# Kernel tuning notes

Measured on AMD Instinct MI355X. Metric: run time of the kernel, lower is better.

The kernel has to match this reference:

```python
import jax, jax.numpy as jnp
import numpy as np

VOC_SIZE = 32768
DIM = 512
NUM_TOPK = 64
BATCH = 4096


def setup_inputs() -> dict:
    key = jax.random.key(0)
    ks = jax.random.split(key, 8)
    lim = 1.0 / np.sqrt(DIM)  # kaiming_uniform(a=sqrt(5)) on [V, d] -> U(-1/sqrt(d), 1/sqrt(d))
    x = jax.random.normal(ks[0], (BATCH, DIM), dtype=jnp.float32)
    codebook = jax.random.uniform(ks[1], (VOC_SIZE, DIM), dtype=jnp.float32, minval=-lim, maxval=lim)
    Wq = jax.random.uniform(ks[2], (DIM, DIM), dtype=jnp.float32, minval=-lim, maxval=lim)
    bq = jax.random.uniform(ks[3], (DIM,), dtype=jnp.float32, minval=-lim, maxval=lim)
    Wk = jax.random.uniform(ks[4], (DIM, DIM), dtype=jnp.float32, minval=-lim, maxval=lim)
    bk = jax.random.uniform(ks[5], (DIM,), dtype=jnp.float32, minval=-lim, maxval=lim)
    Wv = jax.random.uniform(ks[6], (DIM, DIM), dtype=jnp.float32, minval=-lim, maxval=lim)
    bv = jax.random.uniform(ks[7], (DIM,), dtype=jnp.float32, minval=-lim, maxval=lim)
    return {"x": x, "codebook": codebook, "Wq": Wq, "bq": bq,
            "Wk": Wk, "bk": bk, "Wv": Wv, "bv": bv}


def reference(x, codebook, Wq, bq, Wk, bk, Wv, bv):
    # projections (torch Linear with weight stored pre-transposed as [in, out])
    q = x @ Wq + bq              # [B, d]
    k = codebook @ Wk + bk       # [V, d]
    v = codebook @ Wv + bv       # [V, d]

    dots = jnp.einsum('bd,kd->bk', q, k)              # [B, V]
    top, _ = jax.lax.top_k(dots, NUM_TOPK)            # [B, num_topk]
    thresh = top[..., -1:]                            # k-th largest value per row
    mask_value = -jnp.finfo(dots.dtype).max
    dots = jnp.where(dots < thresh, mask_value, dots)
    attn = jax.nn.softmax(dots, axis=-1)              # [B, V]
    out = jnp.einsum('bk,kd->bd', attn, v)            # [B, d]
    return out
```

## Files before the change

kernel.cpp:

```cpp
#include <hip/hip_runtime.h>
#include <cstdint>

#define VOC   32768
#define DIM   512
#define TOPK  64
#define BATCH 4096

#define KSIG     2.45f
#define EPS_SEL  0.012f
#define CAND_CAP 512
#define RES_CAP  256
#define FCAP     1024

typedef unsigned short u16;
typedef __attribute__((ext_vector_type(8))) short bf16x8;
typedef __attribute__((ext_vector_type(4))) float f32x4;

__device__ __forceinline__ u16 f2bf(float f) {
    unsigned u = __float_as_uint(f);
    unsigned r = (u + 0x7FFFu + ((u >> 16) & 1u)) >> 16;
    return (u16)r;
}
__device__ __forceinline__ float bf2f(u16 h) {
    return __uint_as_float(((unsigned)h) << 16);
}
__device__ __forceinline__ unsigned enc16(u16 h) {
    return (h & 0x8000u) ? (unsigned)((u16)~h) : (unsigned)(h | 0x8000u);
}
__device__ __forceinline__ float dec16(unsigned s16) {
    u16 h = (s16 & 0x8000u) ? (u16)(s16 ^ 0x8000u) : (u16)(~s16);
    return bf2f(h);
}

__device__ __forceinline__ void async16(const void* g, void* l) {
    __builtin_amdgcn_global_load_lds(
        (const __attribute__((address_space(1))) void*)g,
        (__attribute__((address_space(3))) void*)l, 16, 0, 0);
}

template <bool BT, bool F64ACC>
__global__ __launch_bounds__(256)
void gemm64(const float* __restrict__ A, const float* __restrict__ B,
            const float* __restrict__ bias, float* __restrict__ C,
            int M, int N, int K)
{
    const int KS = 16;
    __shared__ float As[KS][68];
    __shared__ float Bs[KS][64];

    const int tid = threadIdx.x;
    const int m0 = blockIdx.y * 64;
    const int n0 = blockIdx.x * 64;
    const int ty = tid >> 4;
    const int tx = tid & 15;

    float acc[4][4];
    double acc64[4][4];
#pragma unroll
    for (int i = 0; i < 4; i++)
#pragma unroll
        for (int j = 0; j < 4; j++) { acc[i][j] = 0.f; if (F64ACC) acc64[i][j] = 0.0; }

    for (int kt = 0; kt < K; kt += KS) {
        {
            int row = tid >> 2, kq = tid & 3;
            const float4 av = *(const float4*)(A + (size_t)(m0 + row) * K + kt + kq * 4);
            As[kq * 4 + 0][row] = av.x;
            As[kq * 4 + 1][row] = av.y;
            As[kq * 4 + 2][row] = av.z;
            As[kq * 4 + 3][row] = av.w;
        }
        if (!BT) {
            int krow = tid >> 4, nq = tid & 15;
            *(float4*)&Bs[krow][nq * 4] =
                *(const float4*)(B + (size_t)(kt + krow) * N + n0 + nq * 4);
        } else {
            int nrow = tid >> 2, kq = tid & 3;
            const float4 bv = *(const float4*)(B + (size_t)(n0 + nrow) * K + kt + kq * 4);
            Bs[kq * 4 + 0][nrow] = bv.x;
            Bs[kq * 4 + 1][nrow] = bv.y;
            Bs[kq * 4 + 2][nrow] = bv.z;
            Bs[kq * 4 + 3][nrow] = bv.w;
        }
        __syncthreads();

#pragma unroll
        for (int kk = 0; kk < KS; kk++) {
            float4 a = *(const float4*)&As[kk][ty * 4];
            float4 b = *(const float4*)&Bs[kk][tx * 4];
            float av[4] = {a.x, a.y, a.z, a.w};
            float bv[4] = {b.x, b.y, b.z, b.w};
#pragma unroll
            for (int i = 0; i < 4; i++)
#pragma unroll
                for (int j = 0; j < 4; j++)
                    acc[i][j] += av[i] * bv[j];
        }
        __syncthreads();
        if (F64ACC) {
#pragma unroll
            for (int i = 0; i < 4; i++)
#pragma unroll
                for (int j = 0; j < 4; j++) { acc64[i][j] += (double)acc[i][j]; acc[i][j] = 0.f; }
        }
    }

    float4 bb = make_float4(0.f, 0.f, 0.f, 0.f);
    if (bias) bb = *(const float4*)(bias + n0 + tx * 4);
#pragma unroll
    for (int i = 0; i < 4; i++) {
        float4 o;
        o.x = (F64ACC ? (float)acc64[i][0] : acc[i][0]) + bb.x;
        o.y = (F64ACC ? (float)acc64[i][1] : acc[i][1]) + bb.y;
        o.z = (F64ACC ? (float)acc64[i][2] : acc[i][2]) + bb.z;
        o.w = (F64ACC ? (float)acc64[i][3] : acc[i][3]) + bb.w;
        *(float4*)(C + (size_t)(m0 + ty * 4 + i) * N + n0 + tx * 4) = o;
    }
}

__global__ void bias_fold(const float* __restrict__ bq, const float* __restrict__ Wk,
                          float* __restrict__ bqk)
{
    int j = blockIdx.x * 256 + threadIdx.x;
    if (j >= DIM) return;
    double s = 0.0;
    const float* wr = Wk + (size_t)j * DIM;
    for (int d = 0; d < DIM; d++) s += (double)bq[d] * (double)wr[d];
    bqk[j] = (float)s;
}

__global__ void zero_ws(unsigned* __restrict__ p, int n)
{
    int i = blockIdx.x * 256 + threadIdx.x;
    if (i < n) p[i] = 0u;
}

__global__ __launch_bounds__(256)
void cbar_accum(const float* __restrict__ cb, float* __restrict__ cbarsum)
{
    const int tid = threadIdx.x;
    const int r0 = blockIdx.x * 128;
    float s0 = 0.f, s1 = 0.f;
    for (int r = 0; r < 128; r++) {
        const float* rp = cb + (size_t)(r0 + r) * DIM;
        s0 += rp[tid];
        s1 += rp[tid + 256];
    }
    atomicAdd(&cbarsum[tid], s0);
    atomicAdd(&cbarsum[tid + 256], s1);
}

__global__ __launch_bounds__(256)
void rowstats(const float* __restrict__ q2, const float* __restrict__ cbarsum,
              float* __restrict__ trow, float* __restrict__ sigrow)
{
    const int tid = threadIdx.x, lane = tid & 63, wave = tid >> 6;
    const int row = blockIdx.x * 4 + wave;
    const float* qp = q2 + (size_t)row * DIM + lane * 8;
    float4 a0 = *(const float4*)qp, a1 = *(const float4*)(qp + 4);
    const float* cp = cbarsum + lane * 8;
    float4 c0 = *(const float4*)cp, c1 = *(const float4*)(cp + 4);
    float mu = a0.x*c0.x + a0.y*c0.y + a0.z*c0.z + a0.w*c0.w
             + a1.x*c1.x + a1.y*c1.y + a1.z*c1.z + a1.w*c1.w;
    float nr = a0.x*a0.x + a0.y*a0.y + a0.z*a0.z + a0.w*a0.w
             + a1.x*a1.x + a1.y*a1.y + a1.z*a1.z + a1.w*a1.w;
#pragma unroll
    for (int off = 32; off > 0; off >>= 1) {
        mu += __shfl_down(mu, off);
        nr += __shfl_down(nr, off);
    }
    if (lane == 0) {
        mu *= (1.f / VOC);
        float sig = sqrtf(nr * (1.f / 1536.f));
        trow[row] = mu + KSIG * sig;
        sigrow[row] = sig;
    }
}

__global__ __launch_bounds__(256)
void pack_rows(const float* __restrict__ src, u16* __restrict__ hi,
               u16* __restrict__ lo, int R, int log2R)
{
    int idx = blockIdx.x * 256 + threadIdx.x;
    int c8  = idx >> log2R;
    int row = idx & (R - 1);
    const float* sp = src + (size_t)row * DIM + c8 * 8;
    float xv[8];
    *(float4*)&xv[0] = *(const float4*)sp;
    *(float4*)&xv[4] = *(const float4*)(sp + 4);
    int ks = c8 >> 2, ch = c8 & 3;
    size_t ob = ((size_t)(ks * 4 + ch) * R + row) * 8;
    u16 h[8], l[8];
#pragma unroll
    for (int j = 0; j < 8; j++) {
        h[j] = f2bf(xv[j]);
        l[j] = f2bf(xv[j] - bf2f(h[j]));
    }
    *(uint4*)(hi + ob) = *(const uint4*)h;
    if (lo) *(uint4*)(lo + ob) = *(const uint4*)l;
}

__global__ __launch_bounds__(256)
void pack_bT(const float* __restrict__ W, u16* __restrict__ hi, u16* __restrict__ lo)
{
    int idx = blockIdx.x * 256 + threadIdx.x;
    int n  = idx & (DIM - 1);
    int c8 = idx >> 9;
    int ks = c8 >> 2, ch = c8 & 3;
    size_t ob = ((size_t)(ks * 4 + ch) * DIM + n) * 8;
    u16 h[8], l[8];
#pragma unroll
    for (int j = 0; j < 8; j++) {
        float x = W[(size_t)(c8 * 8 + j) * DIM + n];
        h[j] = f2bf(x);
        l[j] = f2bf(x - bf2f(h[j]));
    }
    *(uint4*)(hi + ob) = *(const uint4*)h;
    *(uint4*)(lo + ob) = *(const uint4*)l;
}

__global__ __launch_bounds__(256, 3)
void mfma_dots(const u16* __restrict__ Ah, const u16* __restrict__ Bh,
               const float* __restrict__ trow, unsigned* __restrict__ candBuf,
               unsigned* __restrict__ counters)
{
    __shared__ u16 lds[3 * 8192];

    const int tid  = threadIdx.x;
    const int lane = tid & 63;
    const int wave = tid >> 6;
    const int wm = wave >> 1, wn = wave & 1;
    const int lr = lane & 15;
    const int q  = lane >> 4;

    const int L   = blockIdx.x;
    const int xcd = L & 7;
    const int j   = L >> 3;
    const int m0  = (xcd * 4 + (j & 3)) * 128;
    const int n0  = (j >> 2) * 128;

    const int a  = wave >> 1;
    const u16* src = a ? Bh : Ah;
    const int rb   = a ? n0 : m0;
    const size_t R = a ? (size_t)VOC : (size_t)BATCH;
    const int i0   = (wave & 1) * 4;

    f32x4 acc[4][4] = {};

#define ISSUE(ks, b)                                                          \
    {                                                                         \
        _Pragma("unroll")                                                     \
        for (int s_ = 0; s_ < 4; s_++) {                                      \
            int i_ = i0 + s_;                                                 \
            const u16* gp_ = src + ((size_t)((ks) * 4 + (i_ >> 1)) * R + rb   \
                                    + (i_ & 1) * 64 + lane) * 8;              \
            async16(gp_, &lds[(b) * 8192 + a * 4096 + i_ * 512 + lane * 8]);  \
        }                                                                     \
    }

    ISSUE(0, 0)
    ISSUE(1, 1)

    for (int s = 0; s < 16; s++) {
        if (s == 15) __builtin_amdgcn_s_waitcnt(0x0F70);
        else         __builtin_amdgcn_s_waitcnt(0x0F74);
        __builtin_amdgcn_s_barrier();
        if (s < 14) {
            int b2 = (s + 2) % 3;
            ISSUE(s + 2, b2)
        }
        const u16* base = &lds[(s % 3) * 8192];

        bf16x8 ah[4];
#pragma unroll
        for (int mt = 0; mt < 4; mt++)
            ah[mt] = *(const bf16x8*)&base[q * 1024 + (wm * 64 + mt * 16 + lr) * 8];
#pragma unroll
        for (int nt = 0; nt < 4; nt++) {
            bf16x8 bh = *(const bf16x8*)&base[4096 + q * 1024 + (wn * 64 + nt * 16 + lr) * 8];
#pragma unroll
            for (int mt = 0; mt < 4; mt++)
                acc[mt][nt] = __builtin_amdgcn_mfma_f32_16x16x32_bf16(ah[mt], bh, acc[mt][nt], 0, 0, 0);
        }
    }
#undef ISSUE

#pragma unroll
    for (int mt = 0; mt < 4; mt++) {
#pragma unroll
        for (int r = 0; r < 4; r++) {
            int rowg = m0 + wm * 64 + mt * 16 + q * 4 + r;
            float tr = trow[rowg];
#pragma unroll
            for (int nt = 0; nt < 4; nt++) {
                float val = acc[mt][nt][r];
                if (val >= tr) {
                    unsigned slot = atomicAdd(&counters[rowg], 1u);
                    if (slot < CAND_CAP) {
                        unsigned s16 = enc16(f2bf(val));
                        candBuf[(size_t)rowg * CAND_CAP + slot] =
                            (s16 << 16) | (unsigned)(n0 + wn * 64 + nt * 16 + lr);
                    }
                }
            }
        }
    }
}

__global__ __launch_bounds__(256, 2)
void mfma_out(const u16* __restrict__ Ah, const u16* __restrict__ Al,
              const u16* __restrict__ Bh, const u16* __restrict__ Bl,
              const float* __restrict__ bias, float* __restrict__ Cout, int Ma)
{
    __shared__ u16 lds[2 * 16384];

    const int tid  = threadIdx.x;
    const int lane = tid & 63;
    const int wave = tid >> 6;
    const int wm = wave >> 1, wn = wave & 1;
    const int m0 = blockIdx.y * 128, n0 = blockIdx.x * 128;
    const int lr = lane & 15;
    const int q  = lane >> 4;

    f32x4 acc[4][4] = {};
    const u16* garr[4] = {Ah, Bh, Al, Bl};
    const int a = wave;
    const u16* src = garr[a];
    const bool isA = (a == 0 || a == 2);
    const int rb = isA ? m0 : n0;
    const size_t R = isA ? (size_t)Ma : (size_t)DIM;

#define VISSUE(ks, b)                                                         \
    {                                                                         \
        _Pragma("unroll")                                                     \
        for (int i_ = 0; i_ < 8; i_++) {                                      \
            const u16* gp_ = src + ((size_t)((ks) * 4 + (i_ >> 1)) * R + rb   \
                                    + (i_ & 1) * 64 + lane) * 8;              \
            async16(gp_, &lds[(b) * 16384 + a * 4096 + i_ * 512 + lane * 8]); \
        }                                                                     \
    }

    VISSUE(0, 0)

    for (int ks = 0; ks < 16; ks++) {
        __syncthreads();
        if (ks < 15) VISSUE(ks + 1, (ks + 1) & 1)
        const u16* base = &lds[(ks & 1) * 16384];

        bf16x8 ah[4], al[4];
#pragma unroll
        for (int mt = 0; mt < 4; mt++) {
            int row = wm * 64 + mt * 16 + lr;
            ah[mt] = *(const bf16x8*)&base[0 * 4096 + q * 1024 + row * 8];
            al[mt] = *(const bf16x8*)&base[2 * 4096 + q * 1024 + row * 8];
        }
#pragma unroll
        for (int nt = 0; nt < 4; nt++) {
            int col = wn * 64 + nt * 16 + lr;
            bf16x8 bh = *(const bf16x8*)&base[1 * 4096 + q * 1024 + col * 8];
            bf16x8 bl = *(const bf16x8*)&base[3 * 4096 + q * 1024 + col * 8];
#pragma unroll
            for (int mt = 0; mt < 4; mt++) {
                acc[mt][nt] = __builtin_amdgcn_mfma_f32_16x16x32_bf16(ah[mt], bh, acc[mt][nt], 0, 0, 0);
                acc[mt][nt] = __builtin_amdgcn_mfma_f32_16x16x32_bf16(ah[mt], bl, acc[mt][nt], 0, 0, 0);
                acc[mt][nt] = __builtin_amdgcn_mfma_f32_16x16x32_bf16(al[mt], bh, acc[mt][nt], 0, 0, 0);
            }
        }
    }
#undef VISSUE

#pragma unroll
    for (int mt = 0; mt < 4; mt++)
#pragma unroll
        for (int nt = 0; nt < 4; nt++) {
            int col = n0 + wn * 64 + nt * 16 + lr;
            float bb = bias[col];
#pragma unroll
            for (int r = 0; r < 4; r++) {
                int rowg = m0 + wm * 64 + mt * 16 + q * 4 + r;
                Cout[(size_t)rowg * DIM + col] = acc[mt][nt][r] + bb;
            }
        }
}

__global__ __launch_bounds__(256)
void select6(const unsigned* __restrict__ candBuf, const unsigned* __restrict__ counters,
             const float* __restrict__ trow, const float* __restrict__ q2,
             const float* __restrict__ codebook, float* __restrict__ y,
             unsigned* __restrict__ flags)
{
    __shared__ unsigned recs[CAND_CAP];
    __shared__ unsigned long long keys[RES_CAP];
    __shared__ float q2s[DIM];
    __shared__ float wArr[RES_CAP];
    __shared__ float redf[256];
    __shared__ unsigned redu[256];
    __shared__ unsigned s_R;

    const int tid  = threadIdx.x;
    const int lane = tid & 63;
    const int wave = tid >> 6;
    const int row  = blockIdx.x;

    const unsigned cnt = counters[row];
    if (cnt < TOPK || cnt > CAND_CAP) {
        if (tid == 0) flags[row] = 1u;
        return;
    }
    for (int i = tid; i < DIM; i += 256) q2s[i] = q2[(size_t)row * DIM + i];
    for (int i = tid; i < CAND_CAP; i += 256)
        recs[i] = (i < (int)cnt) ? candBuf[(size_t)row * CAND_CAP + i] : 0u;
    if (tid == 0) s_R = 0;
    __syncthreads();

    for (int k = 2; k <= CAND_CAP; k <<= 1) {
        for (int j = k >> 1; j > 0; j >>= 1) {
#pragma unroll
            for (int e = 0; e < 2; e++) {
                int i = tid + e * 256;
                int ixj = i ^ j;
                if (ixj > i) {
                    unsigned a = recs[i], b = recs[ixj];
                    if (((i & k) == 0) ? (a < b) : (a > b)) { recs[i] = b; recs[ixj] = a; }
                }
            }
            __syncthreads();
        }
    }

    const float a64  = dec16(recs[TOPK - 1] >> 16);
    const float band = a64 - 2.f * EPS_SEL;
    if (trow[row] > band) {
        if (tid == 0) flags[row] = 1u;
        return;
    }

#pragma unroll
    for (int e = 0; e < 2; e++) {
        int i = tid + e * 256;
        if (i < (int)cnt && dec16(recs[i] >> 16) >= band) atomicAdd(&s_R, 1u);
    }
    __syncthreads();
    const int R = (int)s_R;
    if (R > RES_CAP) {
        if (tid == 0) flags[row] = 1u;
        return;
    }

    for (int c = wave; c < R; c += 4) {
        unsigned idx = recs[c] & 0xFFFFu;
        const float* cb = codebook + (size_t)idx * DIM + lane * 8;
        float4 c0 = *(const float4*)cb, c1 = *(const float4*)(cb + 4);
        const float* qp = &q2s[lane * 8];
        float4 a0 = *(const float4*)qp, a1 = *(const float4*)(qp + 4);
        double s = (double)a0.x * c0.x + (double)a0.y * c0.y
                 + (double)a0.z * c0.z + (double)a0.w * c0.w
                 + (double)a1.x * c1.x + (double)a1.y * c1.y
                 + (double)a1.z * c1.z + (double)a1.w * c1.w;
#pragma unroll
        for (int off = 32; off > 0; off >>= 1) s += __shfl_down(s, off);
        if (lane == 0) {
            float val = (float)s;
            unsigned b = __float_as_uint(val);
            unsigned sk = (b & 0x80000000u) ? ~b : (b | 0x80000000u);
            keys[c] = ((unsigned long long)(~sk) << 32) | idx;
        }
    }
    if (tid >= R && tid < RES_CAP) keys[tid] = ~0ULL;
    __syncthreads();

    for (int k = 2; k <= RES_CAP; k <<= 1) {
        for (int j = k >> 1; j > 0; j >>= 1) {
            int ixj = tid ^ j;
            if (ixj > tid) {
                unsigned long long a = keys[tid], b2 = keys[ixj];
                if (((tid & k) == 0) ? (a > b2) : (a < b2)) { keys[tid] = b2; keys[ixj] = a; }
            }
            __syncthreads();
        }
    }

    const unsigned threshInv = (unsigned)(keys[TOPK - 1] >> 32);
    unsigned sk0 = ~(unsigned)(keys[0] >> 32);
    const float vmax = __uint_as_float((sk0 & 0x80000000u) ? (sk0 & 0x7FFFFFFFu) : ~sk0);

    unsigned hi = (unsigned)(keys[tid] >> 32);
    bool sel = (hi <= threshInv);
    unsigned sk = ~hi;
    float val = __uint_as_float((sk & 0x80000000u) ? (sk & 0x7FFFFFFFu) : ~sk);
    float w = sel ? expf(val - vmax) : 0.f;
    wArr[tid] = w;
    redf[tid] = w;
    redu[tid] = sel ? 1u : 0u;
    __syncthreads();
    for (int s = 128; s > 0; s >>= 1) {
        if (tid < s) { redf[tid] += redf[tid + s]; redu[tid] += redu[tid + s]; }
        __syncthreads();
    }
    const float invZ = 1.0f / redf[0];
    const int selCount = (int)redu[0];

    for (int d = tid; d < DIM; d += 256) {
        float acc = 0.f;
        for (int i = 0; i < selCount; i++) {
            unsigned idx = (unsigned)(keys[i] & 0xFFFFFFFFu);
            acc += wArr[i] * codebook[(size_t)idx * DIM + d];
        }
        y[(size_t)row * DIM + d] = acc * invZ;
    }
}

__global__ __launch_bounds__(256)
void fallback_row(const unsigned* __restrict__ flags, const float* __restrict__ q2,
                  const float* __restrict__ codebook, const float* __restrict__ trow,
                  const float* __restrict__ sigrow, float* __restrict__ y)
{
    const int row = blockIdx.x;
    if (!flags[row]) return;

    __shared__ float q2s[DIM];
    __shared__ unsigned long long keys[FCAP];
    __shared__ float wArr[FCAP];
    __shared__ float redf[256];
    __shared__ unsigned redu[256];
    __shared__ unsigned s_cnt;

    const int tid = threadIdx.x;
    for (int i = tid; i < DIM; i += 256) q2s[i] = q2[(size_t)row * DIM + i];
    const float sig = sigrow[row];
    float tf = trow[row] - 0.35f * sig;
    unsigned cnt = 0;

    for (int it = 0; it < 16; it++) {
        if (tid == 0) s_cnt = 0;
        __syncthreads();
        for (int i = tid; i < VOC; i += 256) {
            const float* cb = codebook + (size_t)i * DIM;
            double s = 0.0;
            for (int d = 0; d < DIM; d += 4) {
                float4 c4 = *(const float4*)(cb + d);
                s += (double)q2s[d + 0] * (double)c4.x + (double)q2s[d + 1] * (double)c4.y
                   + (double)q2s[d + 2] * (double)c4.z + (double)q2s[d + 3] * (double)c4.w;
            }
            float vv = (float)s;
            if (vv >= tf) {
                unsigned p = atomicAdd(&s_cnt, 1u);
                if (p < FCAP) {
                    unsigned b = __float_as_uint(vv);
                    unsigned sk = (b & 0x80000000u) ? ~b : (b | 0x80000000u);
                    keys[p] = ((unsigned long long)(~sk) << 32) | (unsigned)i;
                }
            }
        }
        __syncthreads();
        cnt = s_cnt;
        if (cnt > FCAP) { tf += 0.15f * sig; continue; }
        if (cnt < TOPK) { tf -= 0.35f * sig; continue; }
        break;
    }
    if (cnt > FCAP) cnt = FCAP;
    for (int i = tid; i < FCAP; i += 256)
        if (i >= (int)cnt) keys[i] = ~0ULL;
    __syncthreads();

    for (int k = 2; k <= FCAP; k <<= 1) {
        for (int j = k >> 1; j > 0; j >>= 1) {
#pragma unroll
            for (int e = 0; e < 4; e++) {
                int i = tid + e * 256;
                int ixj = i ^ j;
                if (ixj > i) {
                    unsigned long long a = keys[i], b = keys[ixj];
                    if (((i & k) == 0) ? (a > b) : (a < b)) { keys[i] = b; keys[ixj] = a; }
                }
            }
            __syncthreads();
        }
    }

    const unsigned threshInv = (unsigned)(keys[TOPK - 1] >> 32);
    unsigned sk0 = ~(unsigned)(keys[0] >> 32);
    const float vmax = __uint_as_float((sk0 & 0x80000000u) ? (sk0 & 0x7FFFFFFFu) : ~sk0);

    float lsum = 0.f; unsigned lcnt = 0;
    for (int i = tid; i < FCAP; i += 256) {
        unsigned hi = (unsigned)(keys[i] >> 32);
        bool sel = (hi <= threshInv);
        unsigned sk = ~hi;
        float vv = __uint_as_float((sk & 0x80000000u) ? (sk & 0x7FFFFFFFu) : ~sk);
        float w = sel ? expf(vv - vmax) : 0.f;
        wArr[i] = w;
        lsum += w; lcnt += sel ? 1u : 0u;
    }
    redf[tid] = lsum; redu[tid] = lcnt;
    __syncthreads();
    for (int s = 128; s > 0; s >>= 1) {
        if (tid < s) { redf[tid] += redf[tid + s]; redu[tid] += redu[tid + s]; }
        __syncthreads();
    }
    const float invZ = 1.f / redf[0];
    const int selCount = (int)redu[0];

    for (int d = tid; d < DIM; d += 256) {
        float acc = 0.f;
        for (int i = 0; i < selCount; i++) {
            unsigned idx = (unsigned)(keys[i] & 0xFFFFFFFFu);
            acc += wArr[i] * codebook[(size_t)idx * DIM + d];
        }
        y[(size_t)row * DIM + d] = acc * invZ;
    }
}

extern "C" void kernel_launch(void* const* d_in, const int* in_sizes, int n_in,
                              void* d_out, int out_size, void* d_ws, size_t ws_size,
                              hipStream_t stream)
{
    const float* x        = (const float*)d_in[0];
    const float* codebook = (const float*)d_in[1];
    const float* Wq       = (const float*)d_in[2];
    const float* bq       = (const float*)d_in[3];
    const float* Wk       = (const float*)d_in[4];
    const float* Wv       = (const float*)d_in[6];
    const float* bv       = (const float*)d_in[7];
    float* out = (float*)d_out;

    float* q2   = (float*)d_ws;
    float* Wqk  = q2   + (size_t)BATCH * DIM;
    float* bqk  = Wqk  + (size_t)DIM * DIM;
    float* y    = bqk  + 1024;
    float* trow = y    + (size_t)BATCH * DIM;
    float* sigr = trow + BATCH;
    unsigned* counters = (unsigned*)(sigr + BATCH);
    unsigned* flags    = counters + BATCH;
    float* cbarsum     = (float*)(flags + BATCH);
    unsigned* candBuf  = (unsigned*)(cbarsum + 512);
    u16* q2h = (u16*)(candBuf + (size_t)BATCH * CAND_CAP);
    u16* cbh = q2h + (size_t)BATCH * DIM;
    u16* yh  = cbh + (size_t)VOC * DIM;
    u16* yl  = yh  + (size_t)BATCH * DIM;
    u16* wvh = yl  + (size_t)BATCH * DIM;
    u16* wvl = wvh + (size_t)DIM * DIM;

    dim3 blk(256);

    zero_ws<<<dim3(34), blk, 0, stream>>>(counters, BATCH * 2 + 512);

    gemm64<true, true><<<dim3(DIM / 64, DIM / 64), blk, 0, stream>>>(
        Wq, Wk, nullptr, Wqk, DIM, DIM, DIM);
    bias_fold<<<dim3(2), blk, 0, stream>>>(bq, Wk, bqk);
    gemm64<false, true><<<dim3(DIM / 64, BATCH / 64), blk, 0, stream>>>(
        x, Wqk, bqk, q2, BATCH, DIM, DIM);

    cbar_accum<<<dim3(VOC / 128), blk, 0, stream>>>(codebook, cbarsum);
    rowstats<<<dim3(BATCH / 4), blk, 0, stream>>>(q2, cbarsum, trow, sigr);

    pack_rows<<<dim3(BATCH * 64 / 256), blk, 0, stream>>>(q2, q2h, nullptr, BATCH, 12);
    pack_rows<<<dim3(VOC * 64 / 256), blk, 0, stream>>>(codebook, cbh, nullptr, VOC, 15);
    pack_bT<<<dim3(DIM * 64 / 256), blk, 0, stream>>>(Wv, wvh, wvl);

    mfma_dots<<<dim3(8192), blk, 0, stream>>>(q2h, cbh, trow, candBuf, counters);

    select6<<<dim3(BATCH), blk, 0, stream>>>(
        candBuf, counters, trow, q2, codebook, y, flags);
    fallback_row<<<dim3(BATCH), blk, 0, stream>>>(
        flags, q2, codebook, trow, sigr, y);

    pack_rows<<<dim3(BATCH * 64 / 256), blk, 0, stream>>>(y, yh, yl, BATCH, 12);
    mfma_out<<<dim3(DIM / 128, BATCH / 128), blk, 0, stream>>>(
        yh, yl, wvh, wvl, bv, out, BATCH);
}
```

Baseline: 720.3 us.

## Enlarge dots GEMM tile to 256x256 with 8 waves and 4-stage async pipeline

Replaces the 128x128 tile, 4-wave bf16 MFMA dot kernel with a 256x256 tile, 512-thread kernel. Each wave computes a 128x64 sub-tile. LDS staging becomes a 4-buffer ring with loads split into two halves interleaved with the compute phases, and s_setprio is raised around the MFMA bursts. The larger tile is meant to cut global and LDS traffic per FLOP and hide load latency better. In exchange it uses much more LDS (128KB) and more registers, which lowers occupancy, and the candidate-emission epilogue grows per wave.

```diff
diff --git a/kernel.cpp b/kernel.cpp
--- a/kernel.cpp
+++ b/kernel.cpp
@@ -219,77 +219,102 @@
     *(uint4*)(lo + ob) = *(const uint4*)l;
 }
 
-__global__ __launch_bounds__(256, 3)
-void mfma_dots(const u16* __restrict__ Ah, const u16* __restrict__ Bh,
-               const float* __restrict__ trow, unsigned* __restrict__ candBuf,
-               unsigned* __restrict__ counters)
-{
-    __shared__ u16 lds[3 * 8192];
+__global__ __launch_bounds__(512, 2)
+void mfma_dots256(const u16* __restrict__ Ah, const u16* __restrict__ Bh,
+                  const float* __restrict__ trow, unsigned* __restrict__ candBuf,
+                  unsigned* __restrict__ counters)
+{
+    __shared__ u16 lds[4 * 16384];
 
     const int tid  = threadIdx.x;
     const int lane = tid & 63;
     const int wave = tid >> 6;
-    const int wm = wave >> 1, wn = wave & 1;
+    const int wm = wave >> 2, wn = wave & 3;
     const int lr = lane & 15;
     const int q  = lane >> 4;
 
     const int L   = blockIdx.x;
     const int xcd = L & 7;
     const int j   = L >> 3;
-    const int m0  = (xcd * 4 + (j & 3)) * 128;
-    const int n0  = (j >> 2) * 128;
-
-    const int a  = wave >> 1;
-    const u16* src = a ? Bh : Ah;
-    const int rb   = a ? n0 : m0;
-    const size_t R = a ? (size_t)VOC : (size_t)BATCH;
-    const int i0   = (wave & 1) * 4;
-
-    f32x4 acc[4][4] = {};
-
-#define ISSUE(ks, b)                                                          \
-    {                                                                         \
-        _Pragma("unroll")                                                     \
-        for (int s_ = 0; s_ < 4; s_++) {                                      \
-            int i_ = i0 + s_;                                                 \
-            const u16* gp_ = src + ((size_t)((ks) * 4 + (i_ >> 1)) * R + rb   \
-                                    + (i_ & 1) * 64 + lane) * 8;              \
-            async16(gp_, &lds[(b) * 8192 + a * 4096 + i_ * 512 + lane * 8]);  \
-        }                                                                     \
-    }
-
-    ISSUE(0, 0)
-    ISSUE(1, 1)
-
-    for (int s = 0; s < 16; s++) {
-        if (s == 15) __builtin_amdgcn_s_waitcnt(0x0F70);
-        else         __builtin_amdgcn_s_waitcnt(0x0F74);
+    const int m0  = (xcd * 2 + (j & 1)) * 256;
+    const int n0  = (j >> 1) * 256;
+
+    const bool isA = (wave < 4);
+    const u16* src = isA ? Ah : Bh;
+    const size_t R = isA ? (size_t)BATCH : (size_t)VOC;
+    const int rb   = isA ? m0 : n0;
+    const int ldsB = isA ? 0 : 8192;
+    const int cc   = wave & 3;
+
+#define ISSUE2(t, i0)                                                          \
+    { _Pragma("unroll")                                                        \
+      for (int i_ = (i0); i_ < (i0) + 2; i_++) {                               \
+          const u16* gp_ = src + ((size_t)((t) * 4 + cc) * R + rb              \
+                                  + i_ * 64 + lane) * 8;                       \
+          async16(gp_, &lds[((t) & 3) * 16384 + ldsB                           \
+                            + (cc * 256 + i_ * 64 + lane) * 8]);               \
+      } }
+#define ISSUE4(t) ISSUE2(t, 0) ISSUE2(t, 2)
+
+    f32x4 acc[8][4] = {};
+
+    ISSUE4(0)
+    ISSUE4(1)
+    ISSUE4(2)
+    __builtin_amdgcn_s_waitcnt(0x0F78);
+    __builtin_amdgcn_s_barrier();
+
+    const int aoff = wm * 128;
+    const int boff = wn * 64;
+
+    for (int t = 0; t < 16; t++) {
+        const u16* base = &lds[(t & 3) * 16384];
+
+        if (t < 13) ISSUE2(t + 3, 0)
+        bf16x8 alo[4], bh4[4];
+#pragma unroll
+        for (int mt = 0; mt < 4; mt++)
+            alo[mt] = *(const bf16x8*)&base[(q * 256 + aoff + mt * 16 + lr) * 8];
+#pragma unroll
+        for (int nt = 0; nt < 4; nt++)
+            bh4[nt] = *(const bf16x8*)&base[8192 + (q * 256 + boff + nt * 16 + lr) * 8];
+        __builtin_amdgcn_s_setprio(1);
+#pragma unroll
+        for (int nt = 0; nt < 4; nt++)
+#pragma unroll
+            for (int mt = 0; mt < 4; mt++)
+                acc[mt][nt] = __builtin_amdgcn_mfma_f32_16x16x32_bf16(
+                    alo[mt], bh4[nt], acc[mt][nt], 0, 0, 0);
+        __builtin_amdgcn_s_setprio(0);
         __builtin_amdgcn_s_barrier();
-        if (s < 14) {
-            int b2 = (s + 2) % 3;
-            ISSUE(s + 2, b2)
-        }
-        const u16* base = &lds[(s % 3) * 8192];
-
-        bf16x8 ah[4];
+
+        if (t < 13) ISSUE2(t + 3, 2)
+        bf16x8 ahi[4];
 #pragma unroll
         for (int mt = 0; mt < 4; mt++)
-            ah[mt] = *(const bf16x8*)&base[q * 1024 + (wm * 64 + mt * 16 + lr) * 8];
-#pragma unroll
-        for (int nt = 0; nt < 4; nt++) {
-            bf16x8 bh = *(const bf16x8*)&base[4096 + q * 1024 + (wn * 64 + nt * 16 + lr) * 8];
+            ahi[mt] = *(const bf16x8*)&base[(q * 256 + aoff + 64 + mt * 16 + lr) * 8];
+        __builtin_amdgcn_s_setprio(1);
+#pragma unroll
+        for (int nt = 0; nt < 4; nt++)
 #pragma unroll
             for (int mt = 0; mt < 4; mt++)
-                acc[mt][nt] = __builtin_amdgcn_mfma_f32_16x16x32_bf16(ah[mt], bh, acc[mt][nt], 0, 0, 0);
-        }
-    }
-#undef ISSUE
-
-#pragma unroll
-    for (int mt = 0; mt < 4; mt++) {
+                acc[mt + 4][nt] = __builtin_amdgcn_mfma_f32_16x16x32_bf16(
+                    ahi[mt], bh4[nt], acc[mt + 4][nt], 0, 0, 0);
+        __builtin_amdgcn_s_setprio(0);
+
+        if (t < 13)       __builtin_amdgcn_s_waitcnt(0x0F78);
+        else if (t == 13) __builtin_amdgcn_s_waitcnt(0x0F74);
+        else if (t == 14) __builtin_amdgcn_s_waitcnt(0x0F70);
+        if (t < 15)       __builtin_amdgcn_s_barrier();
+    }
+#undef ISSUE2
+#undef ISSUE4
+
+#pragma unroll
+    for (int mt = 0; mt < 8; mt++) {
 #pragma unroll
         for (int r = 0; r < 4; r++) {
-            int rowg = m0 + wm * 64 + mt * 16 + q * 4 + r;
+            int rowg = m0 + wm * 128 + mt * 16 + q * 4 + r;
             float tr = trow[rowg];
 #pragma unroll
             for (int nt = 0; nt < 4; nt++) {
@@ -658,7 +683,7 @@
     pack_rows<<<dim3(VOC * 64 / 256), blk, 0, stream>>>(codebook, cbh, nullptr, VOC, 15);
     pack_bT<<<dim3(DIM * 64 / 256), blk, 0, stream>>>(Wv, wvh, wvl);
 
-    mfma_dots<<<dim3(8192), blk, 0, stream>>>(q2h, cbh, trow, candBuf, counters);
+    mfma_dots256<<<dim3(2048), dim3(512), 0, stream>>>(q2h, cbh, trow, candBuf, counters);
 
     select6<<<dim3(BATCH), blk, 0, stream>>>(
         candBuf, counters, trow, q2, codebook, y, flags);
```

Measured after the change: 869.3 us. 20.7% more time.

## Enlarge mfma_dots tile to 256x128 with each wave owning 64 full-width rows

Applied to the files above, without the earlier changes.

Changes the dots GEMM block tile from 128x128 to 256x128, so each of the four waves computes a 64x128 strip with 4x8 accumulators. Grid size halves and the per-stage LDS buffer grows to hold 256 A rows and 128 B columns, with all threads cooperating on the async loads. This doubles the arithmetic done per byte loaded and per B fragment read from LDS. In exchange it uses more registers and LDS per block, lowering occupancy from 3 to 2 blocks per CU.

```diff
diff --git a/kernel.cpp b/kernel.cpp
--- a/kernel.cpp
+++ b/kernel.cpp
@@ -219,87 +219,83 @@
     *(uint4*)(lo + ob) = *(const uint4*)l;
 }
 
-__global__ __launch_bounds__(256, 3)
+__global__ __launch_bounds__(256, 2)
 void mfma_dots(const u16* __restrict__ Ah, const u16* __restrict__ Bh,
                const float* __restrict__ trow, unsigned* __restrict__ candBuf,
                unsigned* __restrict__ counters)
 {
-    __shared__ u16 lds[3 * 8192];
+    __shared__ u16 lds[3 * 12288];
 
     const int tid  = threadIdx.x;
     const int lane = tid & 63;
     const int wave = tid >> 6;
-    const int wm = wave >> 1, wn = wave & 1;
     const int lr = lane & 15;
     const int q  = lane >> 4;
 
     const int L   = blockIdx.x;
     const int xcd = L & 7;
     const int j   = L >> 3;
-    const int m0  = (xcd * 4 + (j & 3)) * 128;
-    const int n0  = (j >> 2) * 128;
-
-    const int a  = wave >> 1;
-    const u16* src = a ? Bh : Ah;
-    const int rb   = a ? n0 : m0;
-    const size_t R = a ? (size_t)VOC : (size_t)BATCH;
-    const int i0   = (wave & 1) * 4;
-
-    f32x4 acc[4][4] = {};
-
-#define ISSUE(ks, b)                                                          \
-    {                                                                         \
-        _Pragma("unroll")                                                     \
-        for (int s_ = 0; s_ < 4; s_++) {                                      \
-            int i_ = i0 + s_;                                                 \
-            const u16* gp_ = src + ((size_t)((ks) * 4 + (i_ >> 1)) * R + rb   \
-                                    + (i_ & 1) * 64 + lane) * 8;              \
-            async16(gp_, &lds[(b) * 8192 + a * 4096 + i_ * 512 + lane * 8]);  \
-        }                                                                     \
-    }
-
-    ISSUE(0, 0)
-    ISSUE(1, 1)
+    const int m0  = (xcd * 2 + (j & 1)) * 256;
+    const int n0  = (j >> 1) * 128;
+
+#define ISSUE_T(t)                                                             \
+    { _Pragma("unroll")                                                        \
+      for (int i_ = 0; i_ < 4; i_++) {                                         \
+          int u_ = tid + i_ * 256;                                             \
+          int ch_ = u_ >> 8, r_ = u_ & 255;                                    \
+          const u16* gp_ = Ah + ((size_t)((t) * 4 + ch_) * BATCH + m0 + r_) * 8; \
+          async16(gp_, &lds[((t) % 3) * 12288 + u_ * 8]);                      \
+      }                                                                        \
+      _Pragma("unroll")                                                        \
+      for (int i_ = 0; i_ < 2; i_++) {                                         \
+          int u_ = tid + i_ * 256;                                             \
+          int ch_ = u_ >> 7, c_ = u_ & 127;                                    \
+          const u16* gp_ = Bh + ((size_t)((t) * 4 + ch_) * VOC + n0 + c_) * 8; \
+          async16(gp_, &lds[((t) % 3) * 12288 + 8192 + u_ * 8]);               \
+      } }
+
+    f32x4 acc[4][8] = {};
+
+    ISSUE_T(0)
+    ISSUE_T(1)
 
     for (int s = 0; s < 16; s++) {
         if (s == 15) __builtin_amdgcn_s_waitcnt(0x0F70);
-        else         __builtin_amdgcn_s_waitcnt(0x0F74);
+        else         __builtin_amdgcn_s_waitcnt(0x0F76);
         __builtin_amdgcn_s_barrier();
-        if (s < 14) {
-            int b2 = (s + 2) % 3;
-            ISSUE(s + 2, b2)
-        }
-        const u16* base = &lds[(s % 3) * 8192];
+        if (s < 14) ISSUE_T(s + 2)
+        const u16* base = &lds[(s % 3) * 12288];
 
         bf16x8 ah[4];
 #pragma unroll
         for (int mt = 0; mt < 4; mt++)
-            ah[mt] = *(const bf16x8*)&base[q * 1024 + (wm * 64 + mt * 16 + lr) * 8];
-#pragma unroll
-        for (int nt = 0; nt < 4; nt++) {
-            bf16x8 bh = *(const bf16x8*)&base[4096 + q * 1024 + (wn * 64 + nt * 16 + lr) * 8];
+            ah[mt] = *(const bf16x8*)&base[q * 2048 + (wave * 64 + mt * 16 + lr) * 8];
+#pragma unroll
+        for (int nt = 0; nt < 8; nt++) {
+            bf16x8 bh = *(const bf16x8*)&base[8192 + q * 1024 + (nt * 16 + lr) * 8];
 #pragma unroll
             for (int mt = 0; mt < 4; mt++)
-                acc[mt][nt] = __builtin_amdgcn_mfma_f32_16x16x32_bf16(ah[mt], bh, acc[mt][nt], 0, 0, 0);
-        }
-    }
-#undef ISSUE
+                acc[mt][nt] = __builtin_amdgcn_mfma_f32_16x16x32_bf16(
+                    ah[mt], bh, acc[mt][nt], 0, 0, 0);
+        }
+    }
+#undef ISSUE_T
 
 #pragma unroll
     for (int mt = 0; mt < 4; mt++) {
 #pragma unroll
         for (int r = 0; r < 4; r++) {
-            int rowg = m0 + wm * 64 + mt * 16 + q * 4 + r;
+            int rowg = m0 + wave * 64 + mt * 16 + q * 4 + r;
             float tr = trow[rowg];
 #pragma unroll
-            for (int nt = 0; nt < 4; nt++) {
+            for (int nt = 0; nt < 8; nt++) {
                 float val = acc[mt][nt][r];
                 if (val >= tr) {
                     unsigned slot = atomicAdd(&counters[rowg], 1u);
                     if (slot < CAND_CAP) {
                         unsigned s16 = enc16(f2bf(val));
                         candBuf[(size_t)rowg * CAND_CAP + slot] =
-                            (s16 << 16) | (unsigned)(n0 + wn * 64 + nt * 16 + lr);
+                            (s16 << 16) | (unsigned)(n0 + nt * 16 + lr);
                     }
                 }
             }
@@ -658,7 +654,7 @@
     pack_rows<<<dim3(VOC * 64 / 256), blk, 0, stream>>>(codebook, cbh, nullptr, VOC, 15);
     pack_bT<<<dim3(DIM * 64 / 256), blk, 0, stream>>>(Wv, wvh, wvl);
 
-    mfma_dots<<<dim3(8192), blk, 0, stream>>>(q2h, cbh, trow, candBuf, counters);
+    mfma_dots<<<dim3(4096), blk, 0, stream>>>(q2h, cbh, trow, candBuf, counters);
 
     select6<<<dim3(BATCH), blk, 0, stream>>>(
         candBuf, counters, trow, q2, codebook, y, flags);
```

Result: slower. 769.5 us (+6.8%).
